# Performance work log

Measured on AMD Instinct MI355X. Metric: run time of the kernel, lower is better.

The kernel has to match this reference:

```python
import jax, jax.numpy as jnp
import numpy as np

K = 7            # involution kernel size
GC = 16          # group_channels (canonical involution)
EPS = 1e-6


def ln_cf(x, w, b):
    # channels_first LayerNorm over channel dim (axis=1), as in ConvNeXt utils
    u = jnp.mean(x, axis=1, keepdims=True)
    s = jnp.mean((x - u) ** 2, axis=1, keepdims=True)
    xn = (x - u) / jnp.sqrt(s + EPS)
    return w[:, None, None] * xn + b[:, None, None]


def gelu(x):
    return jax.nn.gelu(x, approximate=False)  # torch nn.GELU default (erf)


def involution(x, w1, b1, w2, b2):
    # x: (B,C,H,W). Kernel-generating head: 1x1 conv -> ReLU -> 1x1 conv.
    B, C, H, W = x.shape
    G = C // GC
    mid = jnp.einsum('bchw,mc->bmhw', x, w1) + b1[None, :, None, None]
    mid = jax.nn.relu(mid)
    wk = jnp.einsum('bmhw,km->bkhw', mid, w2) + b2[None, :, None, None]
    wk = wk.reshape(B, G, K * K, H, W)  # per-pixel, per-group K*K kernels
    pad = (K - 1) // 2
    xp = jnp.pad(x, ((0, 0), (0, 0), (pad, pad), (pad, pad)))
    out = jnp.zeros((B, G, GC, H, W), dtype=x.dtype)
    # accumulate over the K*K spatial offsets (fixed small loop, no big unfold)
    for idx in range(K * K):
        i, j = divmod(idx, K)
        xs = xp[:, :, i:i + H, j:j + W].reshape(B, G, GC, H, W)
        out = out + wk[:, :, idx][:, :, None] * xs
    return out.reshape(B, C, H, W)


def setup_inputs() -> dict:
    key = jax.random.key(0)
    ks = jax.random.split(key, 8)
    B, C, O, H, Wd = 4, 128, 256, 128, 128
    mid = C // 4
    G = C // GC
    sc = 0.05
    return {
        'x': jax.random.normal(ks[0], (B, C, H, Wd), jnp.float32),
        'w1': jax.random.normal(ks[1], (mid, C), jnp.float32) * sc,
        'b1': jnp.zeros((mid,), jnp.float32),
        'w2': jax.random.normal(ks[2], (K * K * G, mid), jnp.float32) * sc,
        'b2': jnp.zeros((K * K * G,), jnp.float32),
        'ln1_w': jnp.ones((C,), jnp.float32),
        'ln1_b': jnp.zeros((C,), jnp.float32),
        'conv_w': jax.random.normal(ks[3], (O, C), jnp.float32) * sc,
        'ln2_w': jnp.ones((O,), jnp.float32),
        'ln2_b': jnp.zeros((O,), jnp.float32),
        'map_w': jax.random.normal(ks[4], (O, C), jnp.float32) * sc,
        'map_b': jnp.zeros((O,), jnp.float32),
        'ln3_w': jnp.ones((O,), jnp.float32),
        'ln3_b': jnp.zeros((O,), jnp.float32),
    }


def reference(x, w1, b1, w2, b2, ln1_w, ln1_b, conv_w, ln2_w, ln2_b,
              map_w, map_b, ln3_w, ln3_b):
    # invblock: Involution -> LayerNorm(channels_first) -> GELU
    x1 = involution(x, w1, b1, w2, b2)
    x1 = gelu(ln_cf(x1, ln1_w, ln1_b))
    # conv_block: 1x1 conv (no bias) -> LayerNorm
    x1 = ln_cf(jnp.einsum('bchw,oc->bohw', x1, conv_w), ln2_w, ln2_b)
    # mapping (channels differ): 1x1 conv (bias) -> LayerNorm
    xm = jnp.einsum('bchw,oc->bohw', x, map_w) + map_b[None, :, None, None]
    xm = ln_cf(xm, ln3_w, ln3_b)
    return gelu(x1 + xm)
```

## Files before the change

kernel.cpp:

```cpp
#include <hip/hip_runtime.h>

typedef unsigned short ushort_t;
typedef unsigned int uint_t;

#define NB 4
#define NC 128
#define NH 128
#define NW 128
#define NPIX 65536
#define NMID 32
#define NKK 49
#define NK 392
#define NKP 400
#define NO 256
#define LN_EPS 1e-6f

typedef __attribute__((ext_vector_type(8))) short short8;
typedef __attribute__((ext_vector_type(4))) float floatx4;
typedef __attribute__((ext_vector_type(2))) float floatx2;

__device__ __forceinline__ float bf2f(ushort_t u) {
    union { uint_t i; float f; } v; v.i = ((uint_t)u) << 16; return v.f;
}
__device__ __forceinline__ float bf2f_lo(uint_t u) {
    union { uint_t i; float f; } v; v.i = u << 16; return v.f;
}
__device__ __forceinline__ float bf2f_hi(uint_t u) {
    union { uint_t i; float f; } v; v.i = u & 0xffff0000u; return v.f;
}
__device__ __forceinline__ floatx2 up2(uint_t u) {
    union { uint_t i; float f; } lo, hi;
    lo.i = u << 16; hi.i = u & 0xffff0000u;
    floatx2 r; r[0] = lo.f; r[1] = hi.f; return r;
}
__device__ __forceinline__ ushort_t f2bf(float f) {
    union { float f; uint_t i; } v; v.f = f;
    uint_t x = v.i;
    uint_t r = (x + 0x7FFFu + ((x >> 16) & 1u)) >> 16;
    return (ushort_t)r;
}
__device__ __forceinline__ float gelu_f(float x) {
    return 0.5f * x * (1.0f + erff(x * 0.70710678118654752f));
}
__device__ __forceinline__ float ldin(const void* p, int i, int isf32) {
    return isf32 ? ((const float*)p)[i] : bf2f(((const ushort_t*)p)[i]);
}
__device__ __forceinline__ void gload_lds16(const void* g, void* l) {
    __builtin_amdgcn_global_load_lds(
        (const __attribute__((address_space(1))) void*)g,
        (__attribute__((address_space(3))) void*)l, 16, 0, 0);
}

__device__ __forceinline__ int sniff_isf32(const void* x, int* lf) {
    int t = threadIdx.x;
    if (t < 64) {
        const uint_t* xw = (const uint_t*)x;
        int cnt = 0;
#pragma unroll
        for (int j = 0; j < 8; j++) {
            uint_t wv = xw[t * 8 + j];
            uint_t e = (wv >> 7) & 0xffu;
            if (e >= 110u && e <= 135u) cnt++;
        }
#pragma unroll
        for (int d = 1; d < 64; d <<= 1) cnt += __shfl_xor(cnt, d);
        if (t == 0) *lf = (cnt < 256) ? 1 : 0;
    }
    __syncthreads();
    return *lf;
}

__global__ void ksentinel(uint_t* __restrict__ out, int nwords) {
    int i = blockIdx.x * 256 + threadIdx.x;
    if (i < nwords) out[i] = 0x40004000u;
}

__global__ __launch_bounds__(256) void kpf(const void* x,
                                           const void* w1, const void* w2,
                                           const void* b1, const void* b2,
                                           const void* ln1w, const void* ln1b,
                                           const void* ln2w, const void* ln2b,
                                           const void* map_b,
                                           const void* ln3w, const void* ln3b,
                                           const void* conv_w, const void* map_w,
                                           ushort_t* __restrict__ xT,
                                           ushort_t* __restrict__ w1b,
                                           ushort_t* __restrict__ w2b,
                                           float* __restrict__ b1f,
                                           float* __restrict__ b2f,
                                           float* __restrict__ ln1wf,
                                           float* __restrict__ ln1bf,
                                           float* __restrict__ ln2wf,
                                           float* __restrict__ ln2bf,
                                           float* __restrict__ mbf,
                                           float* __restrict__ ln3wf,
                                           float* __restrict__ ln3bf,
                                           ushort_t* __restrict__ wfrag) {
    __shared__ __align__(16) ushort_t tile[32][72];
    __shared__ int lf;
    int isf32 = sniff_isf32(x, &lf);
    int bid = blockIdx.x;
    int t = threadIdx.x;

    if (bid < 4096) {
        int b = bid >> 10, h = (bid >> 3) & 127;
        int wchunk = bid & 1, cchunk = (bid >> 1) & 3;
        int w0 = wchunk << 6, c0 = cchunk << 5;
        {
            int cc = t >> 3, wseg = t & 7;
            size_t idx = (size_t)((b * NC + c0 + cc) * NH + h) * NW + w0 + wseg * 8;
            uint4 pk;
            if (isf32) {
                float4 f0 = *(const float4*)((const float*)x + idx);
                float4 f1 = *(const float4*)((const float*)x + idx + 4);
                pk.x = (uint_t)f2bf(f0.x) | ((uint_t)f2bf(f0.y) << 16);
                pk.y = (uint_t)f2bf(f0.z) | ((uint_t)f2bf(f0.w) << 16);
                pk.z = (uint_t)f2bf(f1.x) | ((uint_t)f2bf(f1.y) << 16);
                pk.w = (uint_t)f2bf(f1.z) | ((uint_t)f2bf(f1.w) << 16);
            } else {
                pk = *(const uint4*)((const ushort_t*)x + idx);
            }
            *(uint4*)&tile[cc][wseg * 8] = pk;
        }
        __syncthreads();
        int px = t >> 2, seg = t & 3;
        ushort_t o[8];
#pragma unroll
        for (int j = 0; j < 8; j++) o[j] = tile[seg * 8 + j][px];
        *(uint4*)&xT[((size_t)((b * NH + h) * NW) + w0 + px) * NC + c0 + seg * 8]
            = *(uint4*)o;
    } else if (bid < 4224) {
        int i = (bid - 4096) * 256 + t;
        if (i < NMID * NC) w1b[i] = f2bf(ldin(w1, i, isf32));
        if (i < NKP * NMID) w2b[i] = (i < NK * NMID) ? f2bf(ldin(w2, i, isf32))
                                                     : (ushort_t)0;
        if (i < NMID) b1f[i] = ldin(b1, i, isf32);
        if (i < NKP)  b2f[i] = (i < NK) ? ldin(b2, i, isf32) : 0.f;
        if (i < NC) { ln1wf[i] = ldin(ln1w, i, isf32); ln1bf[i] = ldin(ln1b, i, isf32); }
        if (i < NO) {
            ln2wf[i] = ldin(ln2w, i, isf32); ln2bf[i] = ldin(ln2b, i, isf32);
            mbf[i]   = ldin(map_b, i, isf32);
            ln3wf[i] = ldin(ln3w, i, isf32); ln3bf[i] = ldin(ln3b, i, isf32);
        }
    } else {
        int cid = (bid - 4224) * 256 + t;
        int lane = cid & 63, n4 = (cid >> 6) & 15, br = (cid >> 10) & 1, kb = cid >> 11;
        int o = n4 * 16 + (lane & 15);
        int ch0 = kb * 32 + (lane >> 4) * 8;
        const void* src = br ? map_w : conv_w;
        ushort_t* dst = wfrag + (size_t)cid * 8;
#pragma unroll
        for (int j = 0; j < 8; j++)
            dst[j] = f2bf(ldin(src, o * NC + ch0 + j, isf32));
    }
}

__global__ __launch_bounds__(512) void k1f(const ushort_t* __restrict__ xT,
                                           const ushort_t* __restrict__ w1b,
                                           const float* __restrict__ b1f,
                                           const ushort_t* __restrict__ w2b,
                                           const float* __restrict__ b2f,
                                           const float* __restrict__ ln1wf,
                                           const float* __restrict__ ln1bf,
                                           ushort_t* __restrict__ y1) {
    __shared__ __align__(16) char smem[52800];
    __shared__ ushort_t midbuf[64 * 32];
    ushort_t* wkstage = (ushort_t*)smem;
    uint4*    x8      = (uint4*)smem;
    float*    sred    = (float*)smem;

    int t = threadIdx.x;
    int lane = t & 63;
    int w = __builtin_amdgcn_readfirstlane(t >> 6);
    int l16 = lane & 15, quad = lane >> 4;
    int tileid = blockIdx.x;
    int tilex = tileid & 15, tiley = (tileid >> 4) & 15, b = tileid >> 8;
    int h0 = tiley * 8, w0 = tilex * 8;
    int w4 = w & 3;

    if (w < 4) {
        int lpx = 16 * w + l16;
        int py = lpx >> 3, pxx = lpx & 7;
        const ushort_t* abase = xT + (size_t)((b * NH + h0 + py) * NW + w0 + pxx) * NC + quad * 8;
        floatx4 am0 = (floatx4)0.f, am1 = (floatx4)0.f;
#pragma unroll
        for (int kb = 0; kb < 4; kb++) {
            short8 a   = *(const short8*)(abase + kb * 32);
            short8 b0  = *(const short8*)(w1b + (l16) * NC + kb * 32 + quad * 8);
            short8 b1v = *(const short8*)(w1b + (16 + l16) * NC + kb * 32 + quad * 8);
            am0 = __builtin_amdgcn_mfma_f32_16x16x32_bf16(a, b0, am0, 0, 0, 0);
            am1 = __builtin_amdgcn_mfma_f32_16x16x32_bf16(a, b1v, am1, 0, 0, 0);
        }
        float bia0 = b1f[l16], bia1 = b1f[16 + l16];
#pragma unroll
        for (int r = 0; r < 4; r++) {
            int m = 16 * w + quad * 4 + r;
            midbuf[m * 32 + l16]      = f2bf(fmaxf(am0[r] + bia0, 0.f));
            midbuf[m * 32 + 16 + l16] = f2bf(fmaxf(am1[r] + bia1, 0.f));
        }
    }
    __syncthreads();

    {
        short8 aM = *(const short8*)(midbuf + (16 * w4 + l16) * 32 + quad * 8);
        int nt0 = (w < 4) ? 0 : 13;
        int nt1 = (w < 4) ? 13 : 25;
        for (int nt = nt0; nt < nt1; nt++) {
            int n = nt * 16 + l16;
            short8 bw = *(const short8*)(w2b + n * 32 + quad * 8);
            floatx4 c = __builtin_amdgcn_mfma_f32_16x16x32_bf16(aM, bw, (floatx4)0.f, 0, 0, 0);
            float bias = b2f[n];
#pragma unroll
            for (int r = 0; r < 4; r++)
                wkstage[n * 66 + 16 * w4 + quad * 4 + r] = f2bf(c[r] + bias);
        }
    }
    __syncthreads();

    uint_t wkp[25];
#pragma unroll
    for (int j = 0; j < 24; j++) {
        uint_t lo = wkstage[(w * NKK + 2 * j) * 66 + lane];
        uint_t hi = wkstage[(w * NKK + 2 * j + 1) * 66 + lane];
        wkp[j] = lo | (hi << 16);
    }
    wkp[24] = wkstage[(w * NKK + 48) * 66 + lane];
    __syncthreads();

    for (int it = 0; it < 7; it++) {
        int idx = it * 512 + t;
        if (idx < 3136) {
            int oct = idx & 15, hp = idx >> 4;
            int hy = hp / 14, hx = hp - hy * 14;
            int gh = h0 + hy - 3, gw = w0 + hx - 3;
            uint4 v = make_uint4(0u, 0u, 0u, 0u);
            if ((unsigned)gh < (unsigned)NH && (unsigned)gw < (unsigned)NW) {
                v = *(const uint4*)&xT[(size_t)((b * NH + gh) * NW + gw) * NC + 8 * oct];
            }
            x8[oct * 197 + hp] = v;
        }
    }
    __syncthreads();

    int py = lane >> 3, pxx = lane & 7;
    int base0 = py * 14 + pxx;
    floatx2 a2[8];
#pragma unroll
    for (int j = 0; j < 8; j++) a2[j] = (floatx2)0.f;

#pragma unroll
    for (int tap = 0; tap < NKK; tap++) {
        float wkf = (tap & 1) ? bf2f((ushort_t)(wkp[tap >> 1] >> 16))
                              : bf2f((ushort_t)(wkp[tap >> 1] & 0xffffu));
        floatx2 wk2 = (floatx2)wkf;
        int xa = base0 + (tap / 7) * 14 + (tap % 7);
        uint4 u0 = x8[(2 * w) * 197 + xa];
        uint4 u1 = x8[(2 * w + 1) * 197 + xa];
        a2[0] = wk2 * up2(u0.x) + a2[0];
        a2[1] = wk2 * up2(u0.y) + a2[1];
        a2[2] = wk2 * up2(u0.z) + a2[2];
        a2[3] = wk2 * up2(u0.w) + a2[3];
        a2[4] = wk2 * up2(u1.x) + a2[4];
        a2[5] = wk2 * up2(u1.y) + a2[5];
        a2[6] = wk2 * up2(u1.z) + a2[6];
        a2[7] = wk2 * up2(u1.w) + a2[7];
    }
    __syncthreads();

    float s = 0.f, sq = 0.f;
#pragma unroll
    for (int j = 0; j < 8; j++) {
        float v0 = a2[j][0], v1 = a2[j][1];
        s += v0; sq += v0 * v0;
        s += v1; sq += v1 * v1;
    }
    sred[(w * 64 + lane) * 2]     = s;
    sred[(w * 64 + lane) * 2 + 1] = sq;
    __syncthreads();
    float ts = 0.f, tq = 0.f;
#pragma unroll
    for (int r = 0; r < 8; r++) {
        ts += sred[(r * 64 + lane) * 2];
        tq += sred[(r * 64 + lane) * 2 + 1];
    }
    float mean = ts * (1.0f / NC);
    float var = tq * (1.0f / NC) - mean * mean;
    float rstd = rsqrtf(var + LN_EPS);

    int p = (b * NH + h0 + py) * NW + w0 + pxx;
    uint_t pk[8];
#pragma unroll
    for (int j = 0; j < 8; j++) {
        int c0 = 16 * w + 2 * j;
        float g0 = gelu_f((a2[j][0] - mean) * rstd * ln1wf[c0] + ln1bf[c0]);
        float g1 = gelu_f((a2[j][1] - mean) * rstd * ln1wf[c0 + 1] + ln1bf[c0 + 1]);
        pk[j] = (uint_t)f2bf(g0) | ((uint_t)f2bf(g1) << 16);
    }
    uint4* dst = (uint4*)(y1 + (size_t)p * NC + 16 * w);
    dst[0] = make_uint4(pk[0], pk[1], pk[2], pk[3]);
    dst[1] = make_uint4(pk[4], pk[5], pk[6], pk[7]);
}

__global__ __launch_bounds__(256, 4) void k23(const void* __restrict__ x,
                                              const ushort_t* __restrict__ y1,
                                              const ushort_t* __restrict__ xT,
                                              const ushort_t* __restrict__ wfrag,
                                              const float* __restrict__ mbf,
                                              const float* __restrict__ ln2wf,
                                              const float* __restrict__ ln2bf,
                                              const float* __restrict__ ln3wf,
                                              const float* __restrict__ ln3bf,
                                              void* __restrict__ out) {
    __shared__ __align__(16) char sbuf[32768];
    __shared__ int lf;
    int isf32 = sniff_isf32(x, &lf);

    int t = threadIdx.x;
    int lane = t & 63;
    int w = __builtin_amdgcn_readfirstlane(t >> 6);
    int quad = lane >> 4, l16 = lane & 15;
    int pair = w >> 1;
    int oh   = w & 1;

    int P0 = blockIdx.x * 32;
    int pw = P0 + pair * 16;
    const ushort_t* aYp = y1 + (size_t)(pw + l16) * NC + quad * 8;
    const ushort_t* aXp = xT + (size_t)(pw + l16) * NC + quad * 8;

    {
        const ushort_t* gsrc = wfrag + (size_t)(w * 512 + lane) * 8;
        char* ldst = sbuf + (size_t)(w * 512) * 16;
#pragma unroll
        for (int i = 0; i < 8; i++)
            gload_lds16(gsrc + i * 64 * 8, ldst + i * 64 * 16);
    }
    short8 Ay[4], Ax[4];
#pragma unroll
    for (int kb = 0; kb < 4; kb++) {
        Ay[kb] = *(const short8*)(aYp + kb * 32);
        Ax[kb] = *(const short8*)(aXp + kb * 32);
    }
    __syncthreads();

    floatx4 accC[8], accM[8];
#pragma unroll
    for (int j = 0; j < 8; j++) { accC[j] = (floatx4)0.f; accM[j] = (floatx4)0.f; }

#pragma unroll
    for (int kb = 0; kb < 4; kb++) {
        short8 ay = Ay[kb], ax = Ax[kb];
#pragma unroll
        for (int j = 0; j < 8; j++) {
            int n4 = oh * 8 + j;
            short8 bc = *(const short8*)(sbuf + (size_t)(n4 * 64 + lane) * 16);
            short8 bm = *(const short8*)(sbuf + 16384 + (size_t)(n4 * 64 + lane) * 16);
            accC[j] = __builtin_amdgcn_mfma_f32_16x16x32_bf16(ay, bc, accC[j], 0, 0, 0);
            accM[j] = __builtin_amdgcn_mfma_f32_16x16x32_bf16(ax, bm, accM[j], 0, 0, 0);
        }
        __syncthreads();
        if (kb < 3) {
            const ushort_t* gsrc = wfrag + ((size_t)(kb + 1) * 2048 + w * 512 + lane) * 8;
            char* ldst = sbuf + (size_t)(w * 512) * 16;
#pragma unroll
            for (int i = 0; i < 8; i++)
                gload_lds16(gsrc + i * 64 * 8, ldst + i * 64 * 16);
            __syncthreads();
        }
    }

#pragma unroll
    for (int j = 0; j < 8; j++) {
        float mb = mbf[(oh * 8 + j) * 16 + l16];
#pragma unroll
        for (int r = 0; r < 4; r++) accM[j][r] += mb;
    }

    floatx4 s1 = (floatx4)0.f, q1 = (floatx4)0.f, s2 = (floatx4)0.f, q2 = (floatx4)0.f;
#pragma unroll
    for (int j = 0; j < 8; j++)
#pragma unroll
        for (int r = 0; r < 4; r++) {
            float a = accC[j][r], m = accM[j][r];
            s1[r] += a; q1[r] += a * a;
            s2[r] += m; q2[r] += m * m;
        }
#pragma unroll
    for (int d = 1; d < 16; d <<= 1) {
#pragma unroll
        for (int r = 0; r < 4; r++) {
            s1[r] += __shfl_xor(s1[r], d);
            q1[r] += __shfl_xor(q1[r], d);
            s2[r] += __shfl_xor(s2[r], d);
            q2[r] += __shfl_xor(q2[r], d);
        }
    }

    float* sstat = (float*)sbuf;
    if (l16 == 0) {
#pragma unroll
        for (int r = 0; r < 4; r++) {
            float* sp = sstat + (((pair * 2 + oh) * 16) + quad * 4 + r) * 4;
            sp[0] = s1[r]; sp[1] = q1[r]; sp[2] = s2[r]; sp[3] = q2[r];
        }
    }
    __syncthreads();

    floatx4 mn1, rs1, mn2, rs2;
#pragma unroll
    for (int r = 0; r < 4; r++) {
        const float* op = sstat + (((pair * 2 + (oh ^ 1)) * 16) + quad * 4 + r) * 4;
        float S1 = s1[r] + op[0], Q1 = q1[r] + op[1];
        float S2 = s2[r] + op[2], Q2 = q2[r] + op[3];
        mn1[r] = S1 * (1.0f / NO);
        rs1[r] = rsqrtf(Q1 * (1.0f / NO) - mn1[r] * mn1[r] + LN_EPS);
        mn2[r] = S2 * (1.0f / NO);
        rs2[r] = rsqrtf(Q2 * (1.0f / NO) - mn2[r] * mn2[r] + LN_EPS);
    }

    int batch = pw >> 14;
    int plocal = (pw & 16383) + quad * 4;
#pragma unroll
    for (int j = 0; j < 8; j++) {
        int o = (oh * 8 + j) * 16 + l16;
        float l2w = ln2wf[o], l2b = ln2bf[o];
        float l3w = ln3wf[o], l3b = ln3bf[o];
        float4 gv;
        {
            float v1, v2;
            v1 = (accC[j][0] - mn1[0]) * rs1[0] * l2w + l2b;
            v2 = (accM[j][0] - mn2[0]) * rs2[0] * l3w + l3b;
            gv.x = gelu_f(v1 + v2);
            v1 = (accC[j][1] - mn1[1]) * rs1[1] * l2w + l2b;
            v2 = (accM[j][1] - mn2[1]) * rs2[1] * l3w + l3b;
            gv.y = gelu_f(v1 + v2);
            v1 = (accC[j][2] - mn1[2]) * rs1[2] * l2w + l2b;
            v2 = (accM[j][2] - mn2[2]) * rs2[2] * l3w + l3b;
            gv.z = gelu_f(v1 + v2);
            v1 = (accC[j][3] - mn1[3]) * rs1[3] * l2w + l2b;
            v2 = (accM[j][3] - mn2[3]) * rs2[3] * l3w + l3b;
            gv.w = gelu_f(v1 + v2);
        }
        size_t oi = ((size_t)(batch * NO + o) << 14) + plocal;
        if (isf32) {
            *(float4*)((float*)out + oi) = gv;
        } else {
            uint_t p0 = (uint_t)f2bf(gv.x) | ((uint_t)f2bf(gv.y) << 16);
            uint_t p1 = (uint_t)f2bf(gv.z) | ((uint_t)f2bf(gv.w) << 16);
            *(uint2*)((ushort_t*)out + oi) = make_uint2(p0, p1);
        }
    }
}

extern "C" void kernel_launch(void* const* d_in, const int* in_sizes, int n_in,
                              void* d_out, int out_size, void* d_ws, size_t ws_size,
                              hipStream_t stream) {
    const void* x      = d_in[0];
    const void* w1     = d_in[1];
    const void* b1     = d_in[2];
    const void* w2     = d_in[3];
    const void* b2     = d_in[4];
    const void* ln1w   = d_in[5];
    const void* ln1b   = d_in[6];
    const void* conv_w = d_in[7];
    const void* ln2w   = d_in[8];
    const void* ln2b   = d_in[9];
    const void* map_w  = d_in[10];
    const void* map_b  = d_in[11];
    const void* ln3w   = d_in[12];
    const void* ln3b   = d_in[13];

    char* ws = (char*)d_ws;
    ushort_t* xT    = (ushort_t*)(ws);
    ushort_t* y1    = (ushort_t*)(ws + 16777216);
    ushort_t* wfrag = (ushort_t*)(ws + 33554432);
    ushort_t* w1b   = (ushort_t*)(ws + 33685504);
    ushort_t* w2b   = (ushort_t*)(ws + 33693696);
    float*    b1f   = (float*)(ws + 33719296);
    float*    b2f   = (float*)(ws + 33719424);
    float*    ln1wf = (float*)(ws + 33721024);
    float*    ln1bf = (float*)(ws + 33721536);
    float*    mbf   = (float*)(ws + 33722048);
    float*    ln2wf = (float*)(ws + 33723072);
    float*    ln2bf = (float*)(ws + 33724096);
    float*    ln3wf = (float*)(ws + 33725120);
    float*    ln3bf = (float*)(ws + 33726144);
    const size_t NEED_SMALL = 33727184;

    if (ws_size < NEED_SMALL) {
        int nwords = out_size / 2;
        ksentinel<<<(nwords + 255) / 256, 256, 0, stream>>>((uint_t*)d_out, nwords);
        return;
    }

    kpf<<<4256, 256, 0, stream>>>(x, w1, w2, b1, b2, ln1w, ln1b,
                                  ln2w, ln2b, map_b, ln3w, ln3b,
                                  conv_w, map_w, xT,
                                  w1b, w2b, b1f, b2f, ln1wf, ln1bf,
                                  ln2wf, ln2bf, mbf, ln3wf, ln3bf, wfrag);
    k1f<<<1024, 512, 0, stream>>>(xT, w1b, b1f, w2b, b2f, ln1wf, ln1bf, y1);
    k23<<<NPIX / 32, 256, 0, stream>>>(x, y1, xT, wfrag, mbf,
                                       ln2wf, ln2bf, ln3wf, ln3bf, d_out);
}
```

Measured before the change: 200.3 us.

## Remap involution threads to two adjacent pixels per thread, reusing loaded rows

Each thread now computes two horizontally adjacent pixels for 8 channels, where before it computed one pixel for 16 channels. Each LDS row load of 8 x-values then feeds both pixels' taps, which cuts shared-memory reads per FMA roughly in half. The LayerNorm reduction adds a cross-half-wave shuffle and a padded shared buffer. The trade-off is more registers per thread (49 packed weights plus two accumulator sets), which may lower occupancy.

```diff
diff --git a/kernel.cpp b/kernel.cpp
--- a/kernel.cpp
+++ b/kernel.cpp
@@ -167,7 +167,6 @@
     __shared__ ushort_t midbuf[64 * 32];
     ushort_t* wkstage = (ushort_t*)smem;
     uint4*    x8      = (uint4*)smem;
-    float*    sred    = (float*)smem;
 
     int t = threadIdx.x;
     int lane = t & 63;
@@ -180,8 +179,8 @@
 
     if (w < 4) {
         int lpx = 16 * w + l16;
-        int py = lpx >> 3, pxx = lpx & 7;
-        const ushort_t* abase = xT + (size_t)((b * NH + h0 + py) * NW + w0 + pxx) * NC + quad * 8;
+        int apy = lpx >> 3, apx = lpx & 7;
+        const ushort_t* abase = xT + (size_t)((b * NH + h0 + apy) * NW + w0 + apx) * NC + quad * 8;
         floatx4 am0 = (floatx4)0.f, am1 = (floatx4)0.f;
 #pragma unroll
         for (int kb = 0; kb < 4; kb++) {
@@ -217,14 +216,13 @@
     }
     __syncthreads();
 
-    uint_t wkp[25];
-#pragma unroll
-    for (int j = 0; j < 24; j++) {
-        uint_t lo = wkstage[(w * NKK + 2 * j) * 66 + lane];
-        uint_t hi = wkstage[(w * NKK + 2 * j + 1) * 66 + lane];
-        wkp[j] = lo | (hi << 16);
-    }
-    wkp[24] = wkstage[(w * NKK + 48) * 66 + lane];
+    int gg = t >> 5, pp = t & 31;
+    int py = pp >> 2, ppx = pp & 3;
+    int px0 = py * 8 + 2 * ppx;
+    uint_t wkp[49];
+#pragma unroll
+    for (int k = 0; k < NKK; k++)
+        wkp[k] = *(const uint_t*)&wkstage[(w * NKK + k) * 66 + px0];
     __syncthreads();
 
     for (int it = 0; it < 7; it++) {
@@ -242,63 +240,78 @@
     }
     __syncthreads();
 
-    int py = lane >> 3, pxx = lane & 7;
-    int base0 = py * 14 + pxx;
-    floatx2 a2[8];
-#pragma unroll
-    for (int j = 0; j < 8; j++) a2[j] = (floatx2)0.f;
-
-#pragma unroll
-    for (int tap = 0; tap < NKK; tap++) {
-        float wkf = (tap & 1) ? bf2f((ushort_t)(wkp[tap >> 1] >> 16))
-                              : bf2f((ushort_t)(wkp[tap >> 1] & 0xffffu));
-        floatx2 wk2 = (floatx2)wkf;
-        int xa = base0 + (tap / 7) * 14 + (tap % 7);
-        uint4 u0 = x8[(2 * w) * 197 + xa];
-        uint4 u1 = x8[(2 * w + 1) * 197 + xa];
-        a2[0] = wk2 * up2(u0.x) + a2[0];
-        a2[1] = wk2 * up2(u0.y) + a2[1];
-        a2[2] = wk2 * up2(u0.z) + a2[2];
-        a2[3] = wk2 * up2(u0.w) + a2[3];
-        a2[4] = wk2 * up2(u1.x) + a2[4];
-        a2[5] = wk2 * up2(u1.y) + a2[5];
-        a2[6] = wk2 * up2(u1.z) + a2[6];
-        a2[7] = wk2 * up2(u1.w) + a2[7];
-    }
-    __syncthreads();
-
-    float s = 0.f, sq = 0.f;
-#pragma unroll
-    for (int j = 0; j < 8; j++) {
-        float v0 = a2[j][0], v1 = a2[j][1];
-        s += v0; sq += v0 * v0;
-        s += v1; sq += v1 * v1;
-    }
-    sred[(w * 64 + lane) * 2]     = s;
-    sred[(w * 64 + lane) * 2 + 1] = sq;
-    __syncthreads();
-    float ts = 0.f, tq = 0.f;
+    floatx2 a0[4], a1[4];
+#pragma unroll
+    for (int j = 0; j < 4; j++) { a0[j] = (floatx2)0.f; a1[j] = (floatx2)0.f; }
+
+#pragma unroll
+    for (int dy = 0; dy < 7; dy++) {
+        int xabase = (py + dy) * 14 + 2 * ppx;
+#pragma unroll
+        for (int m = 0; m < 8; m++) {
+            uint4 u = x8[gg * 197 + xabase + m];
+            floatx2 c0 = up2(u.x), c1 = up2(u.y), c2 = up2(u.z), c3 = up2(u.w);
+            if (m < 7) {
+                floatx2 wv = (floatx2)bf2f((ushort_t)(wkp[dy * 7 + m] & 0xffffu));
+                a0[0] = wv * c0 + a0[0];
+                a0[1] = wv * c1 + a0[1];
+                a0[2] = wv * c2 + a0[2];
+                a0[3] = wv * c3 + a0[3];
+            }
+            if (m > 0) {
+                floatx2 wv = (floatx2)bf2f((ushort_t)(wkp[dy * 7 + m - 1] >> 16));
+                a1[0] = wv * c0 + a1[0];
+                a1[1] = wv * c1 + a1[1];
+                a1[2] = wv * c2 + a1[2];
+                a1[3] = wv * c3 + a1[3];
+            }
+        }
+    }
+    __syncthreads();
+
+    float s0 = 0.f, q0 = 0.f, s1 = 0.f, q1 = 0.f;
+#pragma unroll
+    for (int j = 0; j < 4; j++) {
+        float v00 = a0[j][0], v01 = a0[j][1];
+        float v10 = a1[j][0], v11 = a1[j][1];
+        s0 += v00; q0 += v00 * v00; s0 += v01; q0 += v01 * v01;
+        s1 += v10; q1 += v10 * v10; s1 += v11; q1 += v11 * v11;
+    }
+    s0 += __shfl_xor(s0, 32); q0 += __shfl_xor(q0, 32);
+    s1 += __shfl_xor(s1, 32); q1 += __shfl_xor(q1, 32);
+    float* sred = (float*)smem;
+    if ((t & 32) == 0) {
+        float* sp = sred + (w * 32 + pp) * 5;
+        sp[0] = s0; sp[1] = q0; sp[2] = s1; sp[3] = q1;
+    }
+    __syncthreads();
+    float ts0 = 0.f, tq0 = 0.f, ts1 = 0.f, tq1 = 0.f;
 #pragma unroll
     for (int r = 0; r < 8; r++) {
-        ts += sred[(r * 64 + lane) * 2];
-        tq += sred[(r * 64 + lane) * 2 + 1];
-    }
-    float mean = ts * (1.0f / NC);
-    float var = tq * (1.0f / NC) - mean * mean;
-    float rstd = rsqrtf(var + LN_EPS);
-
-    int p = (b * NH + h0 + py) * NW + w0 + pxx;
-    uint_t pk[8];
-#pragma unroll
-    for (int j = 0; j < 8; j++) {
-        int c0 = 16 * w + 2 * j;
-        float g0 = gelu_f((a2[j][0] - mean) * rstd * ln1wf[c0] + ln1bf[c0]);
-        float g1 = gelu_f((a2[j][1] - mean) * rstd * ln1wf[c0 + 1] + ln1bf[c0 + 1]);
-        pk[j] = (uint_t)f2bf(g0) | ((uint_t)f2bf(g1) << 16);
-    }
-    uint4* dst = (uint4*)(y1 + (size_t)p * NC + 16 * w);
-    dst[0] = make_uint4(pk[0], pk[1], pk[2], pk[3]);
-    dst[1] = make_uint4(pk[4], pk[5], pk[6], pk[7]);
+        const float* sp = sred + (r * 32 + pp) * 5;
+        ts0 += sp[0]; tq0 += sp[1]; ts1 += sp[2]; tq1 += sp[3];
+    }
+    float mean0 = ts0 * (1.0f / NC);
+    float rstd0 = rsqrtf(tq0 * (1.0f / NC) - mean0 * mean0 + LN_EPS);
+    float mean1 = ts1 * (1.0f / NC);
+    float rstd1 = rsqrtf(tq1 * (1.0f / NC) - mean1 * mean1 + LN_EPS);
+
+    int pg = (b * NH + h0 + py) * NW + w0 + 2 * ppx;
+    uint_t pk0[4], pk1[4];
+#pragma unroll
+    for (int j = 0; j < 4; j++) {
+        int c0i = gg * 8 + 2 * j;
+        float w0f = ln1wf[c0i], w1f = ln1wf[c0i + 1];
+        float b0f = ln1bf[c0i], b1f_ = ln1bf[c0i + 1];
+        float g00 = gelu_f((a0[j][0] - mean0) * rstd0 * w0f + b0f);
+        float g01 = gelu_f((a0[j][1] - mean0) * rstd0 * w1f + b1f_);
+        float g10 = gelu_f((a1[j][0] - mean1) * rstd1 * w0f + b0f);
+        float g11 = gelu_f((a1[j][1] - mean1) * rstd1 * w1f + b1f_);
+        pk0[j] = (uint_t)f2bf(g00) | ((uint_t)f2bf(g01) << 16);
+        pk1[j] = (uint_t)f2bf(g10) | ((uint_t)f2bf(g11) << 16);
+    }
+    *(uint4*)&y1[(size_t)pg * NC + gg * 8]       = *(uint4*)pk0;
+    *(uint4*)&y1[(size_t)(pg + 1) * NC + gg * 8] = *(uint4*)pk1;
 }
 
 __global__ __launch_bounds__(256, 4) void k23(const void* __restrict__ x,
```

New measurement: 196.7 us. No clear change (-1.8%).
